# Performance work log

Hardware: AMD Instinct MI355X
Metric: run time of the kernel (lower is better)

## Reference

```python
import jax, jax.numpy as jnp
import numpy as np

K = 8192      # codebook_dim
D = 256       # embedding_dim
BETA = 0.25
DECAY = 0.99
EPS = 1e-05


def setup_inputs() -> dict:
    key = jax.random.key(0)
    k1, k2, k3, k4 = jax.random.split(key, 4)
    lim = 1.0 / K
    return {
        "z": jax.random.normal(k1, (8, D, 32, 32), dtype=jnp.float32),
        "embedding": jax.random.uniform(k2, (K, D), minval=-lim, maxval=lim, dtype=jnp.float32),
        "cluster_size": jax.random.uniform(k3, (K,), dtype=jnp.float32),
        "ema_w": jax.random.uniform(k4, (K, D), minval=-lim, maxval=lim, dtype=jnp.float32),
    }


def reference(z, embedding, cluster_size, ema_w):
    # z: [B, C, H, W] -> [B, H, W, C]
    zp = jnp.transpose(z, (0, 2, 3, 1))
    zf = zp.reshape(-1, D)                                  # [N, D]
    # squared L2 distance to each code: ||z||^2 + ||e||^2 - 2 z.e
    d = (jnp.sum(zf * zf, axis=1, keepdims=True)
         + jnp.sum(embedding * embedding, axis=1)
         - 2.0 * jnp.einsum("nd,kd->nk", zf, embedding))    # [N, K]
    idx = jnp.argmin(d, axis=1)                             # [N]
    z_q = embedding[idx].reshape(zp.shape)                  # [B, H, W, C]

    # EMA update (training branch), expressed with segment sums instead of
    # materializing the one-hot [N, K] matrix.
    counts = jax.ops.segment_sum(jnp.ones_like(idx, dtype=zf.dtype), idx, num_segments=K)
    new_cs = cluster_size * DECAY + (1.0 - DECAY) * counts
    n = jnp.sum(new_cs)
    new_cs = (new_cs + EPS) / (n + K * EPS) * n
    dw = jax.ops.segment_sum(zf, idx, num_segments=K)       # encodings.T @ zf
    new_ema_w = ema_w * DECAY + (1.0 - DECAY) * dw
    new_embedding = new_ema_w / new_cs[:, None]

    sg = jax.lax.stop_gradient
    loss = jnp.mean((sg(z_q) - zp) ** 2) + BETA * jnp.mean((z_q - sg(zp)) ** 2)
    # straight-through estimator, back to NCHW
    z_q_out = jnp.transpose(zp + sg(z_q - zp), (0, 3, 1, 2))
    return z_q_out, loss, idx, new_cs, new_ema_w, new_embedding
```

## Files before the change

### kernel.cpp

```cpp
#include <hip/hip_runtime.h>

#define CHW 262144
#define HWD 1024

typedef _Float16 v8h __attribute__((ext_vector_type(8)));
typedef _Float16 v4h __attribute__((ext_vector_type(4)));
typedef float    v4f __attribute__((ext_vector_type(4)));

static const unsigned OFF_ASQ  = 0;
static const unsigned OFF_BSQ  = 8192;
static const unsigned OFF_CNT  = 16384;
static const unsigned OFF_HEAD = 24576;
static const unsigned OFF_SCAL = 32768;
static const unsigned OFF_NXT  = 32776;
static const unsigned OFF_ZF   = 40968;
static const unsigned OFF_BH   = 2138120;

#define GLL(g, l) __builtin_amdgcn_global_load_lds( \
    (const __attribute__((address_space(1))) void*)(g), \
    (__attribute__((address_space(3))) void*)(l), 16, 0, 0)

__global__ __launch_bounds__(256) void k_prep(const float* __restrict__ z,
        const float* __restrict__ emb, float* __restrict__ asq, float* __restrict__ bsq,
        _Float16* __restrict__ Bh, _Float16* __restrict__ Bm,
        _Float16* __restrict__ Ah, _Float16* __restrict__ Am,
        float* __restrict__ zf32, float* __restrict__ zerobase) {
    int bx = blockIdx.x;
    int t = threadIdx.x;
    if (bx < 32) {
        int n = bx * 256 + t;
        const float* p = z + (size_t)(n >> 10) * CHW + (n & 1023);
        float s = 0.f;
        #pragma unroll 8
        for (int c = 0; c < 256; ++c) { float v = p[(size_t)c << 10]; s = fmaf(v, v, s); }
        asq[n] = s;
    } else if (bx < 2080) {
        int w = (bx - 32) * 4 + (t >> 6);
        int lane = t & 63;
        float4 v = *(const float4*)(emb + (size_t)w * 256 + lane * 4);
        float s = v.x * v.x;
        s = fmaf(v.y, v.y, s); s = fmaf(v.z, v.z, s); s = fmaf(v.w, v.w, s);
        #pragma unroll
        for (int m = 1; m < 64; m <<= 1) s += __shfl_xor(s, m, 64);
        if (lane == 0) bsq[w] = s;
        float e0 = v.x * 8192.0f, e1 = v.y * 8192.0f, e2 = v.z * 8192.0f, e3 = v.w * 8192.0f;
        _Float16 h0 = (_Float16)e0, h1 = (_Float16)e1, h2 = (_Float16)e2, h3 = (_Float16)e3;
        v4h hv = {h0, h1, h2, h3};
        v4h mv = {(_Float16)((e0 - (float)h0) * 2048.0f),
                  (_Float16)((e1 - (float)h1) * 2048.0f),
                  (_Float16)((e2 - (float)h2) * 2048.0f),
                  (_Float16)((e3 - (float)h3) * 2048.0f)};
        *(v4h*)(Bh + (size_t)w * 256 + lane * 4) = hv;
        *(v4h*)(Bm + (size_t)w * 256 + lane * 4) = mv;
    } else if (bx < 2592) {
        __shared__ float s[64][65];
        int blk = bx - 2080;
        int hw0 = (blk & 15) * 64;
        int c0  = ((blk >> 4) & 3) * 64;
        int b   = blk >> 6;
        #pragma unroll
        for (int ii = 0; ii < 16; ++ii) {
            int e = t + ii * 256;
            int c = e >> 6, x = e & 63;
            s[c][x] = z[(size_t)b * CHW + (size_t)(c0 + c) * HWD + hw0 + x];
        }
        __syncthreads();
        int n = t & 63, cseg = (t >> 6) * 16;
        _Float16 hbuf[16], mbuf[16];
        float fbuf[16];
        #pragma unroll
        for (int j = 0; j < 16; ++j) {
            float v = s[cseg + j][n];
            _Float16 h = (_Float16)v;
            float r = v - (float)h;
            fbuf[j] = v;
            hbuf[j] = h;
            mbuf[j] = (_Float16)(r * 2048.0f);
        }
        size_t off = ((size_t)b * 1024 + hw0 + n) * 256 + c0 + cseg;
        *(v8h*)(Ah + off)     = *(v8h*)(hbuf);
        *(v8h*)(Ah + off + 8) = *(v8h*)(hbuf + 8);
        *(v8h*)(Am + off)     = *(v8h*)(mbuf);
        *(v8h*)(Am + off + 8) = *(v8h*)(mbuf + 8);
        #pragma unroll
        for (int q = 0; q < 4; ++q)
            *(float4*)(zf32 + off + q * 4) = *(float4*)(fbuf + q * 4);
    } else {
        int idx = (bx - 2592) * 1024 + t * 4;
        *(float4*)(zerobase + idx) = (float4){0.f, 0.f, 0.f, 0.f};
        if (bx == 2607 && t == 0) {
            *(float4*)(zerobase + 16384) = (float4){0.f, 0.f, 0.f, 0.f};
            *(float4*)(zerobase + 16388) = (float4){0.f, 0.f, 0.f, 0.f};
        }
    }
}

__global__ __launch_bounds__(512, 4) void k_main(
        const _Float16* __restrict__ Ah, const _Float16* __restrict__ Am,
        const _Float16* __restrict__ Bh, const _Float16* __restrict__ Bm,
        const float* __restrict__ asq, const float* __restrict__ bsq,
        unsigned* __restrict__ pdk) {
    __shared__ _Float16 lds[32768];
    const int kt = blockIdx.x, nt = blockIdx.y;
    const int n0 = nt * 128, k0 = kt * 128;
    const int t = threadIdx.x;
    const int lane = t & 63, w = t >> 6;
    const int wrow = w >> 1, wcol = w & 1;
    const int lm = lane & 15, quad = lane >> 4;

    v4f acc1[2][4], acc2[2][4];
    #pragma unroll
    for (int i = 0; i < 2; ++i)
        #pragma unroll
        for (int j = 0; j < 4; ++j) { acc1[i][j] = (v4f){0.f,0.f,0.f,0.f}; acc2[i][j] = (v4f){0.f,0.f,0.f,0.f}; }

    const int row0 = t >> 2;
    const int c40 = (t & 3) ^ ((row0 >> 1) & 3);
    const char* gA  = (const char*)Ah + (size_t)(n0 + row0) * 512 + c40 * 16;
    const char* gAm = (const char*)Am + (size_t)(n0 + row0) * 512 + c40 * 16;
    const char* gB  = (const char*)Bh + (size_t)(k0 + row0) * 512 + c40 * 16;
    const char* gBm = (const char*)Bm + (size_t)(k0 + row0) * 512 + c40 * 16;

    int sa[2], sb[4];
    #pragma unroll
    for (int i = 0; i < 2; ++i) {
        int mr = wrow * 32 + i * 16 + lm;
        sa[i] = mr * 32 + ((quad ^ ((mr >> 1) & 3)) * 8);
    }
    #pragma unroll
    for (int j = 0; j < 4; ++j) {
        int nr = wcol * 64 + j * 16 + lm;
        sb[j] = nr * 32 + ((quad ^ ((nr >> 1) & 3)) * 8);
    }

    auto stage = [&](int cb, int buf) {
        const size_t co = (size_t)cb * 64;
        _Float16* l = lds + buf * 16384 + t * 8;
        GLL(gA + co,  l);
        GLL(gAm + co, l + 4096);
        GLL(gB + co,  l + 8192);
        GLL(gBm + co, l + 12288);
    };

    stage(0, 0);
    for (int cb = 0; cb < 8; ++cb) {
        __syncthreads();
        if (cb < 7) stage(cb + 1, (cb + 1) & 1);
        const _Float16* L = lds + (cb & 1) * 16384;

        v8h fa[2], fam[2];
        #pragma unroll
        for (int i = 0; i < 2; ++i) {
            fa[i]  = *(const v8h*)(L + sa[i]);
            fam[i] = *(const v8h*)(L + 4096 + sa[i]);
        }
        #pragma unroll
        for (int jh = 0; jh < 2; ++jh) {
            v8h fb0  = *(const v8h*)(L + 8192 + sb[jh * 2]);
            v8h fb1  = *(const v8h*)(L + 8192 + sb[jh * 2 + 1]);
            v8h fbm0 = *(const v8h*)(L + 12288 + sb[jh * 2]);
            v8h fbm1 = *(const v8h*)(L + 12288 + sb[jh * 2 + 1]);
            #pragma unroll
            for (int i = 0; i < 2; ++i) {
                int j0 = jh * 2;
                acc1[i][j0]     = __builtin_amdgcn_mfma_f32_16x16x32_f16(fa[i],  fb0,  acc1[i][j0], 0, 0, 0);
                acc2[i][j0]     = __builtin_amdgcn_mfma_f32_16x16x32_f16(fa[i],  fbm0, acc2[i][j0], 0, 0, 0);
                acc2[i][j0]     = __builtin_amdgcn_mfma_f32_16x16x32_f16(fam[i], fb0,  acc2[i][j0], 0, 0, 0);
                acc1[i][j0 + 1] = __builtin_amdgcn_mfma_f32_16x16x32_f16(fa[i],  fb1,  acc1[i][j0 + 1], 0, 0, 0);
                acc2[i][j0 + 1] = __builtin_amdgcn_mfma_f32_16x16x32_f16(fa[i],  fbm1, acc2[i][j0 + 1], 0, 0, 0);
                acc2[i][j0 + 1] = __builtin_amdgcn_mfma_f32_16x16x32_f16(fam[i], fb1,  acc2[i][j0 + 1], 0, 0, 0);
            }
        }
    }

    float bvv[4];
    #pragma unroll
    for (int j = 0; j < 4; ++j) bvv[j] = bsq[k0 + wcol * 64 + j * 16 + lm];
    #pragma unroll
    for (int i = 0; i < 2; ++i) {
        #pragma unroll
        for (int r = 0; r < 4; ++r) {
            int m = n0 + wrow * 32 + i * 16 + quad * 4 + r;
            float av_ = asq[m];
            unsigned best = 0xFFFFFFFFu;
            #pragma unroll
            for (int j = 0; j < 4; ++j) {
                float S = fmaf(acc2[i][j][r], 4.8828125e-4f, acc1[i][j][r]) * 1.220703125e-4f;
                float dd = (av_ + bvv[j]) - 2.0f * S;
                float gv = dd - av_;
                int mi = (int)(gv * 65536.0f) + 32768;
                int col = k0 + wcol * 64 + j * 16 + lm;
                unsigned key = ((unsigned)mi << 13) | (unsigned)col;
                best = key < best ? key : best;
            }
            #pragma unroll
            for (int xm = 1; xm < 16; xm <<= 1) {
                unsigned o = __shfl_xor(best, xm, 64);
                best = o < best ? o : best;
            }
            if (lm == 0) pdk[(size_t)m * 128 + kt * 2 + wcol] = best;
        }
    }
}

__global__ __launch_bounds__(256) void k_red(const unsigned* __restrict__ pdk,
        const float* __restrict__ cs, float* __restrict__ out_idx, int* __restrict__ cnt,
        int* __restrict__ head, int* __restrict__ nxt, float* __restrict__ scal) {
    int bx = blockIdx.x;
    int t = threadIdx.x;
    if (bx < 32) {
        float cv = cs[bx * 256 + t];
        #pragma unroll
        for (int m = 1; m < 64; m <<= 1) cv += __shfl_xor(cv, m, 64);
        if ((t & 63) == 0) atomicAdd(scal + 1, cv);
    }
    int n = bx * 4 + (t >> 6);
    int lane = t & 63;
    unsigned a = pdk[(size_t)n * 128 + lane];
    unsigned b = pdk[(size_t)n * 128 + 64 + lane];
    unsigned v = a < b ? a : b;
    #pragma unroll
    for (int m = 1; m < 64; m <<= 1) {
        unsigned o = __shfl_xor(v, m, 64);
        v = o < v ? o : v;
    }
    if (lane == 0) {
        int k = (int)(v & 8191u);
        out_idx[n] = (float)k;
        atomicAdd(cnt + k, 1);
        int old = atomicExch(head + k, n + 1);
        nxt[n] = old;
    }
}

__global__ __launch_bounds__(256) void k_zq(const float* __restrict__ z, const float* __restrict__ emb,
        const float* __restrict__ out_idx, float* __restrict__ out_zq, float* __restrict__ scal) {
    int n0 = blockIdx.x * 64, c00 = blockIdx.y * 64;
    int lane = threadIdx.x & 63, g = threadIdx.x >> 6;
    int n = n0 + lane;
    int b = n >> 10, hw = n & 1023;
    int idxn = (int)out_idx[n];
    const float* zr = z + (size_t)b * CHW + hw;
    const float* er = emb + (size_t)idxn * 256;
    float* oz = out_zq + (size_t)b * CHW + hw;
    float ls = 0.f;
    #pragma unroll
    for (int q = 0; q < 4; ++q) {
        int c = c00 + g * 16 + q * 4;
        float4 e4 = *(const float4*)(er + c);
        float ev[4] = {e4.x, e4.y, e4.z, e4.w};
        #pragma unroll
        for (int r = 0; r < 4; ++r) {
            float zp = zr[(size_t)(c + r) << 10];
            float dif = ev[r] - zp;
            oz[(size_t)(c + r) << 10] = zp + dif;
            ls = fmaf(dif, dif, ls);
        }
    }
    #pragma unroll
    for (int m = 1; m < 64; m <<= 1) ls += __shfl_xor(ls, m, 64);
    __shared__ float red[4];
    if (lane == 0) red[g] = ls;
    __syncthreads();
    if (threadIdx.x == 0) atomicAdd(scal, red[0] + red[1] + red[2] + red[3]);
}

__global__ __launch_bounds__(256) void k_fin(const float* __restrict__ cs, const float* __restrict__ ema,
        const int* __restrict__ head, const int* __restrict__ nxt, const float* __restrict__ zf32,
        const float* __restrict__ scal, const int* __restrict__ cnt,
        float* __restrict__ out_ncs, float* __restrict__ out_ema,
        float* __restrict__ out_emb, float* __restrict__ out_loss) {
    int k = blockIdx.x * 4 + (threadIdx.x >> 6);
    int lane = threadIdx.x & 63;
    float4 dwv = {0.f, 0.f, 0.f, 0.f};
    int cur = head[k];
    while (cur) {
        int n = cur - 1;
        float4 v = *(const float4*)(zf32 + (size_t)n * 256 + lane * 4);
        dwv.x += v.x; dwv.y += v.y; dwv.z += v.z; dwv.w += v.w;
        cur = nxt[n];
    }
    const float C1 = (float)(1.0 - 0.99);
    const float KEPS = (float)(8192 * 1e-5);
    float ncs0v = cs[k] * 0.99f + C1 * (float)cnt[k];
    float nsum = 0.99f * scal[1] + C1 * 8192.0f;
    float ncs = (ncs0v + 1e-5f) / (nsum + KEPS) * nsum;
    if (lane == 0) out_ncs[k] = ncs;
    size_t base = (size_t)k * 256 + lane * 4;
    float4 e4 = *(const float4*)(ema + base);
    float r0 = e4.x * 0.99f + C1 * dwv.x;
    float r1 = e4.y * 0.99f + C1 * dwv.y;
    float r2 = e4.z * 0.99f + C1 * dwv.z;
    float r3 = e4.w * 0.99f + C1 * dwv.w;
    out_ema[base + 0] = r0; out_ema[base + 1] = r1; out_ema[base + 2] = r2; out_ema[base + 3] = r3;
    out_emb[base + 0] = r0 / ncs; out_emb[base + 1] = r1 / ncs;
    out_emb[base + 2] = r2 / ncs; out_emb[base + 3] = r3 / ncs;
    if (blockIdx.x == 0 && threadIdx.x == 0) {
        float m = scal[0] * (1.0f / 2097152.0f);
        out_loss[0] = m + 0.25f * m;
    }
}

extern "C" void kernel_launch(void* const* d_in, const int* in_sizes, int n_in,
                              void* d_out, int out_size, void* d_ws, size_t ws_size,
                              hipStream_t stream) {
    const float* z   = (const float*)d_in[0];
    const float* emb = (const float*)d_in[1];
    const float* cs  = (const float*)d_in[2];
    const float* ema = (const float*)d_in[3];
    float* out = (float*)d_out;
    float* wsf = (float*)d_ws;

    float* asq  = wsf + OFF_ASQ;
    float* bsq  = wsf + OFF_BSQ;
    int*   cnt  = (int*)(wsf + OFF_CNT);
    int*   head = (int*)(wsf + OFF_HEAD);
    float* scal = wsf + OFF_SCAL;
    int*   nxt  = (int*)(wsf + OFF_NXT);
    float* zf32 = wsf + OFF_ZF;
    _Float16* Bh = (_Float16*)(wsf + OFF_BH);

    float* out_zq   = out;
    float* out_loss = out + 2097152;
    float* out_idx  = out + 2097153;
    float* out_ncs  = out + 2105345;
    float* out_ema  = out + 2113537;
    float* out_emb  = out + 4210689;

    unsigned* pdk = (unsigned*)out;
    _Float16* Ah = (_Float16*)(out + 2113540);
    _Float16* Am = (_Float16*)(out + 2113540 + 1048576);
    _Float16* Bm = (_Float16*)(out + 4210692);

    k_prep<<<2608, 256, 0, stream>>>(z, emb, asq, bsq, Bh, Bm, Ah, Am, zf32, wsf + OFF_CNT);
    k_main<<<dim3(64, 64), 512, 0, stream>>>(Ah, Am, Bh, Bm, asq, bsq, pdk);
    k_red<<<2048, 256, 0, stream>>>(pdk, cs, out_idx, cnt, head, nxt, scal);
    k_zq<<<dim3(128, 4), 256, 0, stream>>>(z, emb, out_idx, out_zq, scal);
    k_fin<<<2048, 256, 0, stream>>>(cs, ema, head, nxt, zf32, scal, cnt, out_ncs, out_ema, out_emb, out_loss);
}
```

Before: 247.4 us.

## Fuse argmin reduction into z_q kernel and transpose partial-key layout

Removes the separate k_red launch by folding the final argmin over the partial keys, the index scatter and the cluster-size sum into the z_q kernel. k_main now writes partial keys in a tile-major layout in workspace, so each z_q block can read them with coalesced loads. Each of the four column-blocks recomputes the same argmin redundantly, and only by==0 performs the atomics. This saves one kernel launch and a global round trip of the indices, at the cost of four times the partial-key reads.

Measured after the change: 243.3 us. No clear change (-1.6%).

```diff
diff --git a/kernel.cpp b/kernel.cpp
--- a/kernel.cpp
+++ b/kernel.cpp
@@ -15,6 +15,7 @@
 static const unsigned OFF_NXT  = 32776;
 static const unsigned OFF_ZF   = 40968;
 static const unsigned OFF_BH   = 2138120;
+static const unsigned OFF_PDK  = 3186696;
 
 #define GLL(g, l) __builtin_amdgcn_global_load_lds( \
     (const __attribute__((address_space(1))) void*)(g), \
@@ -176,12 +177,13 @@
     float bvv[4];
     #pragma unroll
     for (int j = 0; j < 4; ++j) bvv[j] = bsq[k0 + wcol * 64 + j * 16 + lm];
+    unsigned* prow = pdk + ((size_t)(nt * 128 + kt * 2 + wcol) << 7);
     #pragma unroll
     for (int i = 0; i < 2; ++i) {
         #pragma unroll
         for (int r = 0; r < 4; ++r) {
-            int m = n0 + wrow * 32 + i * 16 + quad * 4 + r;
-            float av_ = asq[m];
+            int mm = wrow * 32 + i * 16 + quad * 4 + r;
+            float av_ = asq[n0 + mm];
             unsigned best = 0xFFFFFFFFu;
             #pragma unroll
             for (int j = 0; j < 4; ++j) {
@@ -198,48 +200,54 @@
                 unsigned o = __shfl_xor(best, xm, 64);
                 best = o < best ? o : best;
             }
-            if (lm == 0) pdk[(size_t)m * 128 + kt * 2 + wcol] = best;
-        }
-    }
-}
-
-__global__ __launch_bounds__(256) void k_red(const unsigned* __restrict__ pdk,
-        const float* __restrict__ cs, float* __restrict__ out_idx, int* __restrict__ cnt,
-        int* __restrict__ head, int* __restrict__ nxt, float* __restrict__ scal) {
-    int bx = blockIdx.x;
-    int t = threadIdx.x;
-    if (bx < 32) {
-        float cv = cs[bx * 256 + t];
-        #pragma unroll
-        for (int m = 1; m < 64; m <<= 1) cv += __shfl_xor(cv, m, 64);
-        if ((t & 63) == 0) atomicAdd(scal + 1, cv);
-    }
-    int n = bx * 4 + (t >> 6);
-    int lane = t & 63;
-    unsigned a = pdk[(size_t)n * 128 + lane];
-    unsigned b = pdk[(size_t)n * 128 + 64 + lane];
-    unsigned v = a < b ? a : b;
-    #pragma unroll
-    for (int m = 1; m < 64; m <<= 1) {
-        unsigned o = __shfl_xor(v, m, 64);
-        v = o < v ? o : v;
-    }
-    if (lane == 0) {
-        int k = (int)(v & 8191u);
-        out_idx[n] = (float)k;
-        atomicAdd(cnt + k, 1);
-        int old = atomicExch(head + k, n + 1);
-        nxt[n] = old;
-    }
-}
-
-__global__ __launch_bounds__(256) void k_zq(const float* __restrict__ z, const float* __restrict__ emb,
-        const float* __restrict__ out_idx, float* __restrict__ out_zq, float* __restrict__ scal) {
-    int n0 = blockIdx.x * 64, c00 = blockIdx.y * 64;
-    int lane = threadIdx.x & 63, g = threadIdx.x >> 6;
+            if (lm == 0) prow[mm] = best;
+        }
+    }
+}
+
+__global__ __launch_bounds__(256) void k_zqr(const unsigned* __restrict__ pdk,
+        const float* __restrict__ z, const float* __restrict__ emb, const float* __restrict__ cs,
+        float* __restrict__ out_idx, int* __restrict__ cnt,
+        int* __restrict__ head, int* __restrict__ nxt,
+        float* __restrict__ out_zq, float* __restrict__ scal) {
+    const int bx = blockIdx.x, by = blockIdx.y;
+    const int n0 = bx * 64, c00 = by * 64;
+    const int lane = threadIdx.x & 63, g = threadIdx.x >> 6;
+    const int nt = bx >> 1, mb = (bx & 1) * 64;
+
+    unsigned mn = 0xFFFFFFFFu;
+    const unsigned* base = pdk + (((size_t)nt * 128 + g * 32) << 7) + mb + lane;
+    #pragma unroll 8
+    for (int jj = 0; jj < 32; ++jj) {
+        unsigned key = base[jj << 7];
+        mn = key < mn ? key : mn;
+    }
+    __shared__ unsigned part[4][64];
+    part[g][lane] = mn;
+    __syncthreads();
+    unsigned k0v = part[0][lane], k1v = part[1][lane];
+    unsigned k2v = part[2][lane], k3v = part[3][lane];
+    unsigned f01 = k0v < k1v ? k0v : k1v;
+    unsigned f23 = k2v < k3v ? k2v : k3v;
+    unsigned fkey = f01 < f23 ? f01 : f23;
+    int idxn = (int)(fkey & 8191u);
     int n = n0 + lane;
+
+    if (by == 0) {
+        if (g == 0) {
+            out_idx[n] = (float)idxn;
+            atomicAdd(cnt + idxn, 1);
+            int old = atomicExch(head + idxn, n + 1);
+            nxt[n] = old;
+        } else if (g == 1) {
+            float cv = cs[n];
+            #pragma unroll
+            for (int m = 1; m < 64; m <<= 1) cv += __shfl_xor(cv, m, 64);
+            if (lane == 0) atomicAdd(scal + 1, cv);
+        }
+    }
+
     int b = n >> 10, hw = n & 1023;
-    int idxn = (int)out_idx[n];
     const float* zr = z + (size_t)b * CHW + hw;
     const float* er = emb + (size_t)idxn * 256;
     float* oz = out_zq + (size_t)b * CHW + hw;
@@ -319,6 +327,7 @@
     int*   nxt  = (int*)(wsf + OFF_NXT);
     float* zf32 = wsf + OFF_ZF;
     _Float16* Bh = (_Float16*)(wsf + OFF_BH);
+    unsigned* pdk = (unsigned*)(wsf + OFF_PDK);
 
     float* out_zq   = out;
     float* out_loss = out + 2097152;
@@ -327,14 +336,12 @@
     float* out_ema  = out + 2113537;
     float* out_emb  = out + 4210689;
 
-    unsigned* pdk = (unsigned*)out;
     _Float16* Ah = (_Float16*)(out + 2113540);
     _Float16* Am = (_Float16*)(out + 2113540 + 1048576);
     _Float16* Bm = (_Float16*)(out + 4210692);
 
     k_prep<<<2608, 256, 0, stream>>>(z, emb, asq, bsq, Bh, Bm, Ah, Am, zf32, wsf + OFF_CNT);
     k_main<<<dim3(64, 64), 512, 0, stream>>>(Ah, Am, Bh, Bm, asq, bsq, pdk);
-    k_red<<<2048, 256, 0, stream>>>(pdk, cs, out_idx, cnt, head, nxt, scal);
-    k_zq<<<dim3(128, 4), 256, 0, stream>>>(z, emb, out_idx, out_zq, scal);
+    k_zqr<<<dim3(128, 4), 256, 0, stream>>>(pdk, z, emb, cs, out_idx, cnt, head, nxt, out_zq, scal);
     k_fin<<<2048, 256, 0, stream>>>(cs, ema, head, nxt, zf32, scal, cnt, out_ncs, out_ema, out_emb, out_loss);
 }
```
